# Kernel optimization log

Measured on AMD Instinct MI355X. Metric: run time of the kernel, lower is better.

The kernel has to match this reference:

```python
import jax, jax.numpy as jnp
import numpy as np

# Product-key memory config (matches init_kwargs)
HEADS = 4
K_DIM = 512          # per-head query/key dim; split in two halves of 256
HALF = K_DIM // 2
V_DIM = 512
SUBSIZE = 512        # sub-keys per bank; value table size = SUBSIZE**2
SIZE = SUBSIZE * SUBSIZE
TOPK = 8
TEMP = 1.0
B, T = 4, 2048


def setup_inputs() -> dict:
    key = jax.random.key(0)
    kq, kk, kv = jax.random.split(key, 3)
    bound = 1.0 / np.sqrt(K_DIM)  # reset_parameters: uniform(-1/sqrt(k_dim), 1/sqrt(k_dim))
    query = jax.random.normal(kq, (B, T, HEADS * K_DIM), dtype=jnp.float32)
    keys = jax.random.uniform(kk, (2 * HEADS * SUBSIZE, HALF), dtype=jnp.float32,
                              minval=-bound, maxval=bound)
    # reset_parameters: normal(0, v_dim**-0.5)
    values = jax.random.normal(kv, (SIZE, V_DIM), dtype=jnp.float32) * (V_DIM ** -0.5)
    return {"query": query, "keys": keys, "values": values}


def reference(query, keys, values):
    """retrieve_values: product-key two-stage topk + softmax-weighted embedding bag.
    query: [B, T, HEADS*K_DIM]; keys: [2*HEADS*SUBSIZE, HALF]; values: [SIZE, V_DIM]
    returns retrieved values [B*T, V_DIM].
    """
    Bq, Tq = query.shape[:2]
    N = Bq * Tq
    q = query.reshape(N, HEADS, K_DIM)
    q1, q2 = q[..., :HALF], q[..., HALF:]
    k = keys.reshape(2, HEADS, SUBSIZE, HALF)

    # Sub-key score matmuls (the two 'cdist-like' searches)
    s1 = jnp.einsum('nhd,hsd->nhs', q1, k[0])       # [N, H, SUBSIZE]
    s2 = jnp.einsum('nhd,hsd->nhs', q2, k[1])       # [N, H, SUBSIZE]

    ts1, ti1 = jax.lax.top_k(s1, TOPK)               # [N, H, TOPK]
    ts2, ti2 = jax.lax.top_k(s2, TOPK)

    # Cartesian combination of the two topk sets, then global topk
    comb = (ts1[..., :, None] + ts2[..., None, :]).reshape(N, HEADS, TOPK * TOPK)
    scores, flat_idx = jax.lax.top_k(comb, TOPK)     # [N, H, TOPK]
    sel1 = jnp.take_along_axis(ti1, flat_idx // TOPK, axis=-1)
    sel2 = jnp.take_along_axis(ti2, flat_idx % TOPK, axis=-1)
    indices = sel1 * SUBSIZE + sel2                  # global value-table indices [N, H, TOPK]

    # score_transform: softmax over heads*topk (score_nonlinear='softmax')
    w = jax.nn.softmax(scores.reshape(N, HEADS * TOPK) / TEMP, axis=-1)

    # xformers_embedding_bag: weighted gather-sum over the huge value table
    gathered = values[indices.reshape(N, HEADS * TOPK)]   # [N, H*TOPK, V_DIM]
    vals = jnp.einsum('nk,nkd->nd', w, gathered)          # [N, V_DIM]
    return vals
```

## Files before the change

### kernel.cpp

```cpp
#include <hip/hip_runtime.h>
#include <hip/hip_bf16.h>
#include <math.h>

typedef unsigned short u16;
typedef __attribute__((ext_vector_type(8))) short short8;
typedef __attribute__((ext_vector_type(4))) float f32x4;

#define N_TOK   8192
#define N_HEADS 4
#define KDIM    512
#define HALFD   256
#define VDIM    512
#define SUBK    512
#define NCAND   16

__device__ __forceinline__ u16 f2bf(float f) {
    unsigned u = __float_as_uint(f);
    u += 0x7fffu + ((u >> 16) & 1u);
    return (u16)(u >> 16);
}

__device__ __forceinline__ unsigned med3u(unsigned a, unsigned b, unsigned c) {
    unsigned d;
    asm("v_med3_u32 %0, %1, %2, %3" : "=v"(d) : "v"(a), "v"(b), "v"(c));
    return d;
}

__global__ void k_convert(const float* __restrict__ in, u16* __restrict__ out, int n4) {
    int i = blockIdx.x * blockDim.x + threadIdx.x;
    int stride = gridDim.x * blockDim.x;
    for (; i < n4; i += stride) {
        float4 v = ((const float4*)in)[i];
        unsigned a = (unsigned)f2bf(v.x) | ((unsigned)f2bf(v.y) << 16);
        unsigned b = (unsigned)f2bf(v.z) | ((unsigned)f2bf(v.w) << 16);
        ((uint2*)out)[i] = make_uint2(a, b);
    }
}

__global__ __launch_bounds__(256) void k_score_topk(
    const float* __restrict__ query,
    const u16* __restrict__ kb,
    int* __restrict__ cand)
{
    __shared__ unsigned sc[16 * 513];
    const int nb = blockIdx.x, h = blockIdx.y, half = blockIdx.z;
    const int tid = threadIdx.x;
    const int wave = tid >> 6, l = tid & 63;
    const int lr = l & 15, lk = l >> 4;

    const float* qbase = query + (size_t)(nb * 16 + lr) * (N_HEADS * KDIM)
                       + h * KDIM + half * HALFD + lk * 8;
    short8 a[8];
#pragma unroll
    for (int kf = 0; kf < 8; ++kf) {
        float4 q0 = *(const float4*)(qbase + kf * 32);
        float4 q1 = *(const float4*)(qbase + kf * 32 + 4);
        short8 t;
        t[0] = (short)f2bf(q0.x); t[1] = (short)f2bf(q0.y);
        t[2] = (short)f2bf(q0.z); t[3] = (short)f2bf(q0.w);
        t[4] = (short)f2bf(q1.x); t[5] = (short)f2bf(q1.y);
        t[6] = (short)f2bf(q1.z); t[7] = (short)f2bf(q1.w);
        a[kf] = t;
    }

    const u16* kbase = kb + (size_t)(half * N_HEADS + h) * SUBK * HALFD;
#pragma unroll
    for (int t = 0; t < 8; ++t) {
        const int st = wave * 8 + t;
        const u16* kp = kbase + (size_t)(st * 16 + lr) * HALFD + lk * 8;
        short8 b[8];
#pragma unroll
        for (int kf = 0; kf < 8; ++kf)
            b[kf] = *(const short8*)(kp + kf * 32);
        f32x4 acc = {0.f, 0.f, 0.f, 0.f};
#pragma unroll
        for (int kf = 0; kf < 8; ++kf)
            acc = __builtin_amdgcn_mfma_f32_16x16x32_bf16(a[kf], b[kf], acc, 0, 0, 0);
#pragma unroll
        for (int r = 0; r < 4; ++r) {
            unsigned ub = __float_as_uint(acc[r]);
            unsigned key = ub ^ ((unsigned)((int)ub >> 31) | 0x80000000u);
            key = (key & 0xFFFFFE00u) | (unsigned)(st * 16 + lr);
            sc[(lk * 4 + r) * 513 + st * 16 + lr] = key;
        }
    }
    __syncthreads();

    const int row = tid >> 4, sub = tid & 15;
    unsigned tv[NCAND];
#pragma unroll
    for (int j = 0; j < NCAND; ++j) tv[j] = 0u;
    const int base = row * 513 + sub;
#pragma unroll
    for (int t = 0; t < 32; ++t) {
        unsigned v = sc[base + (t << 4)];
#pragma unroll
        for (int j = NCAND - 1; j >= 1; --j)
            tv[j] = med3u(tv[j - 1], tv[j], v);
        tv[0] = (tv[0] > v) ? tv[0] : v;
    }

    unsigned keep = 0;
#pragma unroll
    for (int r = 0; r < NCAND; ++r) {
        unsigned w = tv[0];
#pragma unroll
        for (int d = 1; d < 16; d <<= 1) {
            unsigned o = __shfl_xor(w, d, 16);
            w = (o > w) ? o : w;
        }
        if (sub == r) keep = w;
        bool pop = (tv[0] == w);
#pragma unroll
        for (int j = 0; j < NCAND - 1; ++j) tv[j] = pop ? tv[j + 1] : tv[j];
        tv[NCAND - 1] = pop ? 0u : tv[NCAND - 1];
    }
    const int n = nb * 16 + row;
    cand[((size_t)n * 8 + (h * 2 + half)) * NCAND + sub] = (int)(keep & 0x1FFu);
}

__global__ __launch_bounds__(256) void k_select_gather(
    const float* __restrict__ query,
    const float* __restrict__ keys,
    const float* __restrict__ values,
    const int* __restrict__ cand,
    float* __restrict__ out)
{
    __shared__ double rv[8][16];
    __shared__ int    ri[8][16];
    __shared__ double tsv[8][8];
    __shared__ int    tsi[8][8];
    __shared__ double s_comb[32];
    __shared__ int    sgi[32];
    __shared__ float  wsm[32];
    __shared__ float  part[4][512];

    const int n = blockIdx.x;
    const int tid = threadIdx.x;

    {
        const int dot = tid >> 1, pt = tid & 1;
        const int g = dot >> 4, j = dot & 15;
        const int h = g >> 1, half = g & 1;
        const int sidx = cand[((size_t)n * 8 + g) * NCAND + j];
        const float* qrow = query + (size_t)n * (N_HEADS * KDIM) + h * KDIM + half * HALFD + pt * 128;
        const float* krow = keys + ((size_t)(half * N_HEADS + h) * SUBK + sidx) * HALFD + pt * 128;
        double a0 = 0, a1 = 0, a2 = 0, a3 = 0;
#pragma unroll 8
        for (int d = 0; d < 128; d += 4) {
            float4 qv = *(const float4*)(qrow + d);
            float4 kv = *(const float4*)(krow + d);
            a0 = fma((double)qv.x, (double)kv.x, a0);
            a1 = fma((double)qv.y, (double)kv.y, a1);
            a2 = fma((double)qv.z, (double)kv.z, a2);
            a3 = fma((double)qv.w, (double)kv.w, a3);
        }
        double s = (a0 + a1) + (a2 + a3);
        double o = __shfl_xor(s, 1);
        if (pt == 0) { rv[g][j] = s + o; ri[g][j] = sidx; }
    }
    __syncthreads();

    if (tid < 128) {
        const int g = tid >> 4, j = tid & 15;
        double v = rv[g][j];
        const int idx = ri[g][j];
        for (int r = 0; r < 8; ++r) {
            double bv = v; int bj = j;
#pragma unroll
            for (int d = 1; d < 16; d <<= 1) {
                double ov = __shfl_xor(bv, d, 16);
                int    oj = __shfl_xor(bj, d, 16);
                if (ov > bv || (ov == bv && oj < bj)) { bv = ov; bj = oj; }
            }
            int widx = __shfl(idx, bj, 16);
            if (j == r) { tsv[g][r] = bv; tsi[g][r] = widx; }
            if (j == bj) v = -1e300;
        }
    }
    __syncthreads();

    {
        const int h = tid >> 6, f = tid & 63;
        double c = tsv[h * 2][f >> 3] + tsv[h * 2 + 1][f & 7];
        for (int r = 0; r < 8; ++r) {
            double bv = c; int bf = f;
#pragma unroll
            for (int d = 1; d < 64; d <<= 1) {
                double ov = __shfl_xor(bv, d, 64);
                int    of = __shfl_xor(bf, d, 64);
                if (ov > bv || (ov == bv && of < bf)) { bv = ov; bf = of; }
            }
            if (f == r) {
                s_comb[h * 8 + r] = bv;
                sgi[h * 8 + r] = tsi[h * 2][bf >> 3] * SUBK + tsi[h * 2 + 1][bf & 7];
            }
            if (f == bf) c = -1e300;
        }
    }
    __syncthreads();

    if (tid < 32) {
        const int k = tid;
        double s = s_comb[k];
        double m = s;
#pragma unroll
        for (int d = 1; d < 32; d <<= 1) m = fmax(m, __shfl_xor(m, d, 32));
        float e = expf((float)(s - m));
        float sum = e;
#pragma unroll
        for (int d = 1; d < 32; d <<= 1) sum += __shfl_xor(sum, d, 32);
        wsm[k] = e / sum;
    }
    __syncthreads();

    {
        const int w = tid >> 6, lane = tid & 63;
        float4 acc0 = {0.f, 0.f, 0.f, 0.f};
        float4 acc1 = {0.f, 0.f, 0.f, 0.f};
#pragma unroll
        for (int b = 0; b < 2; ++b) {
            float4 v0[4], v1[4];
#pragma unroll
            for (int r = 0; r < 4; ++r) {
                const int k = w * 8 + b * 4 + r;
                const float* vr = values + (size_t)sgi[k] * VDIM;
                v0[r] = *(const float4*)(vr + lane * 4);
                v1[r] = *(const float4*)(vr + 256 + lane * 4);
            }
#pragma unroll
            for (int r = 0; r < 4; ++r) {
                const float wk = wsm[w * 8 + b * 4 + r];
                acc0.x = fmaf(wk, v0[r].x, acc0.x);
                acc0.y = fmaf(wk, v0[r].y, acc0.y);
                acc0.z = fmaf(wk, v0[r].z, acc0.z);
                acc0.w = fmaf(wk, v0[r].w, acc0.w);
                acc1.x = fmaf(wk, v1[r].x, acc1.x);
                acc1.y = fmaf(wk, v1[r].y, acc1.y);
                acc1.z = fmaf(wk, v1[r].z, acc1.z);
                acc1.w = fmaf(wk, v1[r].w, acc1.w);
            }
        }
        *(float4*)(&part[w][lane * 4]) = acc0;
        *(float4*)(&part[w][256 + lane * 4]) = acc1;
    }
    __syncthreads();

    {
        const int c = tid * 2;
        float s0 = part[0][c]     + part[1][c]     + part[2][c]     + part[3][c];
        float s1 = part[0][c + 1] + part[1][c + 1] + part[2][c + 1] + part[3][c + 1];
        ((float2*)(out + (size_t)n * VDIM))[tid] = make_float2(s0, s1);
    }
}

extern "C" void kernel_launch(void* const* d_in, const int* in_sizes, int n_in,
                              void* d_out, int out_size, void* d_ws, size_t ws_size,
                              hipStream_t stream) {
    const float* query  = (const float*)d_in[0];
    const float* keys   = (const float*)d_in[1];
    const float* values = (const float*)d_in[2];
    float* out = (float*)d_out;

    char* ws = (char*)d_ws;
    u16* kb   = (u16*)ws;
    int* cand = (int*)(ws + 2097152);

    k_convert<<<512, 256, 0, stream>>>(keys, kb, (2 * N_HEADS * SUBK * HALFD) / 4);

    dim3 gB(N_TOK / 16, N_HEADS, 2);
    k_score_topk<<<gB, 256, 0, stream>>>(query, kb, cand);

    k_select_gather<<<N_TOK, 256, 0, stream>>>(query, keys, values, cand, out);
}
```

Measured before the change: 387.8 us.

## Split select and gather into separate kernels with one wave per token

Moves the weighted value gather out of the per-token select kernel into its own kernel. In the new kernel each 64-lane wave handles one token, takes indices and weights through shuffles, and keeps 16 row loads in flight. This drops the shared-memory partial reduction and the barriers, and lets the gather run at its own occupancy. The cost is an extra launch and a small round trip of indices and weights through global memory.

```diff
diff --git a/kernel.cpp b/kernel.cpp
--- a/kernel.cpp
+++ b/kernel.cpp
@@ -119,12 +119,12 @@
     cand[((size_t)n * 8 + (h * 2 + half)) * NCAND + sub] = (int)(keep & 0x1FFu);
 }
 
-__global__ __launch_bounds__(256) void k_select_gather(
+__global__ __launch_bounds__(256) void k_select(
     const float* __restrict__ query,
     const float* __restrict__ keys,
-    const float* __restrict__ values,
     const int* __restrict__ cand,
-    float* __restrict__ out)
+    int* __restrict__ gout,
+    float* __restrict__ wout)
 {
     __shared__ double rv[8][16];
     __shared__ int    ri[8][16];
@@ -132,8 +132,6 @@
     __shared__ int    tsi[8][8];
     __shared__ double s_comb[32];
     __shared__ int    sgi[32];
-    __shared__ float  wsm[32];
-    __shared__ float  part[4][512];
 
     const int n = blockIdx.x;
     const int tid = threadIdx.x;
@@ -210,48 +208,54 @@
         float sum = e;
 #pragma unroll
         for (int d = 1; d < 32; d <<= 1) sum += __shfl_xor(sum, d, 32);
-        wsm[k] = e / sum;
-    }
-    __syncthreads();
-
-    {
-        const int w = tid >> 6, lane = tid & 63;
-        float4 acc0 = {0.f, 0.f, 0.f, 0.f};
-        float4 acc1 = {0.f, 0.f, 0.f, 0.f};
-#pragma unroll
-        for (int b = 0; b < 2; ++b) {
-            float4 v0[4], v1[4];
-#pragma unroll
-            for (int r = 0; r < 4; ++r) {
-                const int k = w * 8 + b * 4 + r;
-                const float* vr = values + (size_t)sgi[k] * VDIM;
-                v0[r] = *(const float4*)(vr + lane * 4);
-                v1[r] = *(const float4*)(vr + 256 + lane * 4);
-            }
-#pragma unroll
-            for (int r = 0; r < 4; ++r) {
-                const float wk = wsm[w * 8 + b * 4 + r];
-                acc0.x = fmaf(wk, v0[r].x, acc0.x);
-                acc0.y = fmaf(wk, v0[r].y, acc0.y);
-                acc0.z = fmaf(wk, v0[r].z, acc0.z);
-                acc0.w = fmaf(wk, v0[r].w, acc0.w);
-                acc1.x = fmaf(wk, v1[r].x, acc1.x);
-                acc1.y = fmaf(wk, v1[r].y, acc1.y);
-                acc1.z = fmaf(wk, v1[r].z, acc1.z);
-                acc1.w = fmaf(wk, v1[r].w, acc1.w);
-            }
-        }
-        *(float4*)(&part[w][lane * 4]) = acc0;
-        *(float4*)(&part[w][256 + lane * 4]) = acc1;
-    }
-    __syncthreads();
-
-    {
-        const int c = tid * 2;
-        float s0 = part[0][c]     + part[1][c]     + part[2][c]     + part[3][c];
-        float s1 = part[0][c + 1] + part[1][c + 1] + part[2][c + 1] + part[3][c + 1];
-        ((float2*)(out + (size_t)n * VDIM))[tid] = make_float2(s0, s1);
-    }
+        wout[(size_t)n * 32 + k] = e / sum;
+        gout[(size_t)n * 32 + k] = sgi[k];
+    }
+}
+
+__global__ __launch_bounds__(256) void k_gather(
+    const float* __restrict__ values,
+    const int* __restrict__ gidx,
+    const float* __restrict__ w,
+    float* __restrict__ out)
+{
+    const int tok = blockIdx.x * 4 + (threadIdx.x >> 6);
+    const int lane = threadIdx.x & 63;
+
+    float wv = 0.f; unsigned off = 0u;
+    if (lane < 32) {
+        wv  = w[(size_t)tok * 32 + lane];
+        off = (unsigned)gidx[(size_t)tok * 32 + lane] * (unsigned)VDIM;
+    }
+
+    float4 acc0 = {0.f, 0.f, 0.f, 0.f};
+    float4 acc1 = {0.f, 0.f, 0.f, 0.f};
+#pragma unroll
+    for (int kb = 0; kb < 32; kb += 8) {
+        float4 v0[8], v1[8];
+#pragma unroll
+        for (int r = 0; r < 8; ++r) {
+            unsigned o = (unsigned)__shfl((int)off, kb + r, 64);
+            const float* vr = values + (size_t)o;
+            v0[r] = *(const float4*)(vr + lane * 4);
+            v1[r] = *(const float4*)(vr + 256 + lane * 4);
+        }
+#pragma unroll
+        for (int r = 0; r < 8; ++r) {
+            const float wk = __shfl(wv, kb + r, 64);
+            acc0.x = fmaf(wk, v0[r].x, acc0.x);
+            acc0.y = fmaf(wk, v0[r].y, acc0.y);
+            acc0.z = fmaf(wk, v0[r].z, acc0.z);
+            acc0.w = fmaf(wk, v0[r].w, acc0.w);
+            acc1.x = fmaf(wk, v1[r].x, acc1.x);
+            acc1.y = fmaf(wk, v1[r].y, acc1.y);
+            acc1.z = fmaf(wk, v1[r].z, acc1.z);
+            acc1.w = fmaf(wk, v1[r].w, acc1.w);
+        }
+    }
+    float* orow = out + (size_t)tok * VDIM;
+    *(float4*)(orow + lane * 4) = acc0;
+    *(float4*)(orow + 256 + lane * 4) = acc1;
 }
 
 extern "C" void kernel_launch(void* const* d_in, const int* in_sizes, int n_in,
@@ -263,13 +267,16 @@
     float* out = (float*)d_out;
 
     char* ws = (char*)d_ws;
-    u16* kb   = (u16*)ws;
-    int* cand = (int*)(ws + 2097152);
+    u16* kb    = (u16*)ws;
+    int* cand  = (int*)(ws + 2097152);
+    int* gidxb = (int*)(ws + 2097152 + 4194304);
+    float* wb  = (float*)(ws + 2097152 + 4194304 + 1048576);
 
     k_convert<<<512, 256, 0, stream>>>(keys, kb, (2 * N_HEADS * SUBK * HALFD) / 4);
 
     dim3 gB(N_TOK / 16, N_HEADS, 2);
     k_score_topk<<<gB, 256, 0, stream>>>(query, kb, cand);
 
-    k_select_gather<<<N_TOK, 256, 0, stream>>>(query, keys, values, cand, out);
-}
+    k_select<<<N_TOK, 256, 0, stream>>>(query, keys, cand, gidxb, wb);
+    k_gather<<<N_TOK / 4, 256, 0, stream>>>(values, gidxb, wb, out);
+}
```

After: 416.3 us. +7.4%, slower.

## Fuse score/top-k and select/gather kernels into one per-16-token kernel

Applied to the files above, without the earlier changes.

Merges the sub-key scoring and candidate top-k kernel with the rescoring, softmax and value-gather kernel. Each block handles 16 tokens: it loops over the 8 head/half groups to build candidates in shared memory, then processes the 16 tokens one after another. This removes the global candidate buffer round trip and one launch. In exchange the grid shrinks to 512 blocks, and the latency-bound gather phase is serialized per token inside a block, which greatly cuts memory-level parallelism and occupancy.

```diff
diff --git a/kernel.cpp b/kernel.cpp
--- a/kernel.cpp
+++ b/kernel.cpp
@@ -37,95 +37,15 @@
     }
 }
 
-__global__ __launch_bounds__(256) void k_score_topk(
+__global__ __launch_bounds__(256, 2) void k_fused(
     const float* __restrict__ query,
-    const u16* __restrict__ kb,
-    int* __restrict__ cand)
+    const u16*  __restrict__ kb,
+    const float* __restrict__ keys,
+    const float* __restrict__ values,
+    float* __restrict__ out)
 {
     __shared__ unsigned sc[16 * 513];
-    const int nb = blockIdx.x, h = blockIdx.y, half = blockIdx.z;
-    const int tid = threadIdx.x;
-    const int wave = tid >> 6, l = tid & 63;
-    const int lr = l & 15, lk = l >> 4;
-
-    const float* qbase = query + (size_t)(nb * 16 + lr) * (N_HEADS * KDIM)
-                       + h * KDIM + half * HALFD + lk * 8;
-    short8 a[8];
-#pragma unroll
-    for (int kf = 0; kf < 8; ++kf) {
-        float4 q0 = *(const float4*)(qbase + kf * 32);
-        float4 q1 = *(const float4*)(qbase + kf * 32 + 4);
-        short8 t;
-        t[0] = (short)f2bf(q0.x); t[1] = (short)f2bf(q0.y);
-        t[2] = (short)f2bf(q0.z); t[3] = (short)f2bf(q0.w);
-        t[4] = (short)f2bf(q1.x); t[5] = (short)f2bf(q1.y);
-        t[6] = (short)f2bf(q1.z); t[7] = (short)f2bf(q1.w);
-        a[kf] = t;
-    }
-
-    const u16* kbase = kb + (size_t)(half * N_HEADS + h) * SUBK * HALFD;
-#pragma unroll
-    for (int t = 0; t < 8; ++t) {
-        const int st = wave * 8 + t;
-        const u16* kp = kbase + (size_t)(st * 16 + lr) * HALFD + lk * 8;
-        short8 b[8];
-#pragma unroll
-        for (int kf = 0; kf < 8; ++kf)
-            b[kf] = *(const short8*)(kp + kf * 32);
-        f32x4 acc = {0.f, 0.f, 0.f, 0.f};
-#pragma unroll
-        for (int kf = 0; kf < 8; ++kf)
-            acc = __builtin_amdgcn_mfma_f32_16x16x32_bf16(a[kf], b[kf], acc, 0, 0, 0);
-#pragma unroll
-        for (int r = 0; r < 4; ++r) {
-            unsigned ub = __float_as_uint(acc[r]);
-            unsigned key = ub ^ ((unsigned)((int)ub >> 31) | 0x80000000u);
-            key = (key & 0xFFFFFE00u) | (unsigned)(st * 16 + lr);
-            sc[(lk * 4 + r) * 513 + st * 16 + lr] = key;
-        }
-    }
-    __syncthreads();
-
-    const int row = tid >> 4, sub = tid & 15;
-    unsigned tv[NCAND];
-#pragma unroll
-    for (int j = 0; j < NCAND; ++j) tv[j] = 0u;
-    const int base = row * 513 + sub;
-#pragma unroll
-    for (int t = 0; t < 32; ++t) {
-        unsigned v = sc[base + (t << 4)];
-#pragma unroll
-        for (int j = NCAND - 1; j >= 1; --j)
-            tv[j] = med3u(tv[j - 1], tv[j], v);
-        tv[0] = (tv[0] > v) ? tv[0] : v;
-    }
-
-    unsigned keep = 0;
-#pragma unroll
-    for (int r = 0; r < NCAND; ++r) {
-        unsigned w = tv[0];
-#pragma unroll
-        for (int d = 1; d < 16; d <<= 1) {
-            unsigned o = __shfl_xor(w, d, 16);
-            w = (o > w) ? o : w;
-        }
-        if (sub == r) keep = w;
-        bool pop = (tv[0] == w);
-#pragma unroll
-        for (int j = 0; j < NCAND - 1; ++j) tv[j] = pop ? tv[j + 1] : tv[j];
-        tv[NCAND - 1] = pop ? 0u : tv[NCAND - 1];
-    }
-    const int n = nb * 16 + row;
-    cand[((size_t)n * 8 + (h * 2 + half)) * NCAND + sub] = (int)(keep & 0x1FFu);
-}
-
-__global__ __launch_bounds__(256) void k_select_gather(
-    const float* __restrict__ query,
-    const float* __restrict__ keys,
-    const float* __restrict__ values,
-    const int* __restrict__ cand,
-    float* __restrict__ out)
-{
+    __shared__ int    cnd[8][16][NCAND];
     __shared__ double rv[8][16];
     __shared__ int    ri[8][16];
     __shared__ double tsv[8][8];
@@ -135,122 +55,203 @@
     __shared__ float  wsm[32];
     __shared__ float  part[4][512];
 
-    const int n = blockIdx.x;
+    const int nb = blockIdx.x;
     const int tid = threadIdx.x;
-
-    {
-        const int dot = tid >> 1, pt = tid & 1;
-        const int g = dot >> 4, j = dot & 15;
+    const int wave = tid >> 6, l = tid & 63;
+    const int lr = l & 15, lk = l >> 4;
+
+    for (int g = 0; g < 8; ++g) {
         const int h = g >> 1, half = g & 1;
-        const int sidx = cand[((size_t)n * 8 + g) * NCAND + j];
-        const float* qrow = query + (size_t)n * (N_HEADS * KDIM) + h * KDIM + half * HALFD + pt * 128;
-        const float* krow = keys + ((size_t)(half * N_HEADS + h) * SUBK + sidx) * HALFD + pt * 128;
-        double a0 = 0, a1 = 0, a2 = 0, a3 = 0;
+
+        const float* qbase = query + (size_t)(nb * 16 + lr) * (N_HEADS * KDIM)
+                           + h * KDIM + half * HALFD + lk * 8;
+        short8 a[8];
+#pragma unroll
+        for (int kf = 0; kf < 8; ++kf) {
+            float4 q0 = *(const float4*)(qbase + kf * 32);
+            float4 q1 = *(const float4*)(qbase + kf * 32 + 4);
+            short8 t;
+            t[0] = (short)f2bf(q0.x); t[1] = (short)f2bf(q0.y);
+            t[2] = (short)f2bf(q0.z); t[3] = (short)f2bf(q0.w);
+            t[4] = (short)f2bf(q1.x); t[5] = (short)f2bf(q1.y);
+            t[6] = (short)f2bf(q1.z); t[7] = (short)f2bf(q1.w);
+            a[kf] = t;
+        }
+
+        const u16* kbase = kb + (size_t)(half * N_HEADS + h) * SUBK * HALFD;
+#pragma unroll
+        for (int t = 0; t < 8; ++t) {
+            const int st = wave * 8 + t;
+            const u16* kp = kbase + (size_t)(st * 16 + lr) * HALFD + lk * 8;
+            short8 b[8];
+#pragma unroll
+            for (int kf = 0; kf < 8; ++kf)
+                b[kf] = *(const short8*)(kp + kf * 32);
+            f32x4 acc = {0.f, 0.f, 0.f, 0.f};
+#pragma unroll
+            for (int kf = 0; kf < 8; ++kf)
+                acc = __builtin_amdgcn_mfma_f32_16x16x32_bf16(a[kf], b[kf], acc, 0, 0, 0);
+#pragma unroll
+            for (int r = 0; r < 4; ++r) {
+                unsigned ub = __float_as_uint(acc[r]);
+                unsigned key = ub ^ ((unsigned)((int)ub >> 31) | 0x80000000u);
+                key = (key & 0xFFFFFE00u) | (unsigned)(st * 16 + lr);
+                sc[(lk * 4 + r) * 513 + st * 16 + lr] = key;
+            }
+        }
+        __syncthreads();
+
+        const int row = tid >> 4, sub = tid & 15;
+        unsigned tv[NCAND];
+#pragma unroll
+        for (int j = 0; j < NCAND; ++j) tv[j] = 0u;
+        const int base = row * 513 + sub;
+#pragma unroll
+        for (int t = 0; t < 32; ++t) {
+            unsigned v = sc[base + (t << 4)];
+#pragma unroll
+            for (int j = NCAND - 1; j >= 1; --j)
+                tv[j] = med3u(tv[j - 1], tv[j], v);
+            tv[0] = (tv[0] > v) ? tv[0] : v;
+        }
+
+        unsigned keep = 0;
+#pragma unroll
+        for (int r = 0; r < NCAND; ++r) {
+            unsigned w = tv[0];
+#pragma unroll
+            for (int d = 1; d < 16; d <<= 1) {
+                unsigned o = __shfl_xor(w, d, 16);
+                w = (o > w) ? o : w;
+            }
+            if (sub == r) keep = w;
+            bool pop = (tv[0] == w);
+#pragma unroll
+            for (int j = 0; j < NCAND - 1; ++j) tv[j] = pop ? tv[j + 1] : tv[j];
+            tv[NCAND - 1] = pop ? 0u : tv[NCAND - 1];
+        }
+        cnd[g][row][sub] = (int)(keep & 0x1FFu);
+        __syncthreads();
+    }
+
+    for (int tt = 0; tt < 16; ++tt) {
+        const int n = nb * 16 + tt;
+
+        {
+            const int dot = tid >> 1, pt = tid & 1;
+            const int g = dot >> 4, j = dot & 15;
+            const int h = g >> 1, half = g & 1;
+            const int sidx = cnd[g][tt][j];
+            const float* qrow = query + (size_t)n * (N_HEADS * KDIM) + h * KDIM + half * HALFD + pt * 128;
+            const float* krow = keys + ((size_t)(half * N_HEADS + h) * SUBK + sidx) * HALFD + pt * 128;
+            double a0 = 0, a1 = 0, a2 = 0, a3 = 0;
 #pragma unroll 8
-        for (int d = 0; d < 128; d += 4) {
-            float4 qv = *(const float4*)(qrow + d);
-            float4 kv = *(const float4*)(krow + d);
-            a0 = fma((double)qv.x, (double)kv.x, a0);
-            a1 = fma((double)qv.y, (double)kv.y, a1);
-            a2 = fma((double)qv.z, (double)kv.z, a2);
-            a3 = fma((double)qv.w, (double)kv.w, a3);
-        }
-        double s = (a0 + a1) + (a2 + a3);
-        double o = __shfl_xor(s, 1);
-        if (pt == 0) { rv[g][j] = s + o; ri[g][j] = sidx; }
-    }
-    __syncthreads();
-
-    if (tid < 128) {
-        const int g = tid >> 4, j = tid & 15;
-        double v = rv[g][j];
-        const int idx = ri[g][j];
-        for (int r = 0; r < 8; ++r) {
-            double bv = v; int bj = j;
-#pragma unroll
-            for (int d = 1; d < 16; d <<= 1) {
-                double ov = __shfl_xor(bv, d, 16);
-                int    oj = __shfl_xor(bj, d, 16);
-                if (ov > bv || (ov == bv && oj < bj)) { bv = ov; bj = oj; }
-            }
-            int widx = __shfl(idx, bj, 16);
-            if (j == r) { tsv[g][r] = bv; tsi[g][r] = widx; }
-            if (j == bj) v = -1e300;
-        }
-    }
-    __syncthreads();
-
-    {
-        const int h = tid >> 6, f = tid & 63;
-        double c = tsv[h * 2][f >> 3] + tsv[h * 2 + 1][f & 7];
-        for (int r = 0; r < 8; ++r) {
-            double bv = c; int bf = f;
-#pragma unroll
-            for (int d = 1; d < 64; d <<= 1) {
-                double ov = __shfl_xor(bv, d, 64);
-                int    of = __shfl_xor(bf, d, 64);
-                if (ov > bv || (ov == bv && of < bf)) { bv = ov; bf = of; }
-            }
-            if (f == r) {
-                s_comb[h * 8 + r] = bv;
-                sgi[h * 8 + r] = tsi[h * 2][bf >> 3] * SUBK + tsi[h * 2 + 1][bf & 7];
-            }
-            if (f == bf) c = -1e300;
-        }
-    }
-    __syncthreads();
-
-    if (tid < 32) {
-        const int k = tid;
-        double s = s_comb[k];
-        double m = s;
-#pragma unroll
-        for (int d = 1; d < 32; d <<= 1) m = fmax(m, __shfl_xor(m, d, 32));
-        float e = expf((float)(s - m));
-        float sum = e;
-#pragma unroll
-        for (int d = 1; d < 32; d <<= 1) sum += __shfl_xor(sum, d, 32);
-        wsm[k] = e / sum;
-    }
-    __syncthreads();
-
-    {
-        const int w = tid >> 6, lane = tid & 63;
-        float4 acc0 = {0.f, 0.f, 0.f, 0.f};
-        float4 acc1 = {0.f, 0.f, 0.f, 0.f};
-#pragma unroll
-        for (int b = 0; b < 2; ++b) {
-            float4 v0[4], v1[4];
-#pragma unroll
-            for (int r = 0; r < 4; ++r) {
-                const int k = w * 8 + b * 4 + r;
-                const float* vr = values + (size_t)sgi[k] * VDIM;
-                v0[r] = *(const float4*)(vr + lane * 4);
-                v1[r] = *(const float4*)(vr + 256 + lane * 4);
-            }
-#pragma unroll
-            for (int r = 0; r < 4; ++r) {
-                const float wk = wsm[w * 8 + b * 4 + r];
-                acc0.x = fmaf(wk, v0[r].x, acc0.x);
-                acc0.y = fmaf(wk, v0[r].y, acc0.y);
-                acc0.z = fmaf(wk, v0[r].z, acc0.z);
-                acc0.w = fmaf(wk, v0[r].w, acc0.w);
-                acc1.x = fmaf(wk, v1[r].x, acc1.x);
-                acc1.y = fmaf(wk, v1[r].y, acc1.y);
-                acc1.z = fmaf(wk, v1[r].z, acc1.z);
-                acc1.w = fmaf(wk, v1[r].w, acc1.w);
-            }
-        }
-        *(float4*)(&part[w][lane * 4]) = acc0;
-        *(float4*)(&part[w][256 + lane * 4]) = acc1;
-    }
-    __syncthreads();
-
-    {
-        const int c = tid * 2;
-        float s0 = part[0][c]     + part[1][c]     + part[2][c]     + part[3][c];
-        float s1 = part[0][c + 1] + part[1][c + 1] + part[2][c + 1] + part[3][c + 1];
-        ((float2*)(out + (size_t)n * VDIM))[tid] = make_float2(s0, s1);
+            for (int d = 0; d < 128; d += 4) {
+                float4 qv = *(const float4*)(qrow + d);
+                float4 kv = *(const float4*)(krow + d);
+                a0 = fma((double)qv.x, (double)kv.x, a0);
+                a1 = fma((double)qv.y, (double)kv.y, a1);
+                a2 = fma((double)qv.z, (double)kv.z, a2);
+                a3 = fma((double)qv.w, (double)kv.w, a3);
+            }
+            double s = (a0 + a1) + (a2 + a3);
+            double o = __shfl_xor(s, 1);
+            if (pt == 0) { rv[g][j] = s + o; ri[g][j] = sidx; }
+        }
+        __syncthreads();
+
+        if (tid < 128) {
+            const int g = tid >> 4, j = tid & 15;
+            double v = rv[g][j];
+            const int idx = ri[g][j];
+            for (int r = 0; r < 8; ++r) {
+                double bv = v; int bj = j;
+#pragma unroll
+                for (int d = 1; d < 16; d <<= 1) {
+                    double ov = __shfl_xor(bv, d, 16);
+                    int    oj = __shfl_xor(bj, d, 16);
+                    if (ov > bv || (ov == bv && oj < bj)) { bv = ov; bj = oj; }
+                }
+                int widx = __shfl(idx, bj, 16);
+                if (j == r) { tsv[g][r] = bv; tsi[g][r] = widx; }
+                if (j == bj) v = -1e300;
+            }
+        }
+        __syncthreads();
+
+        {
+            const int h = tid >> 6, f = tid & 63;
+            double c = tsv[h * 2][f >> 3] + tsv[h * 2 + 1][f & 7];
+            for (int r = 0; r < 8; ++r) {
+                double bv = c; int bf = f;
+#pragma unroll
+                for (int d = 1; d < 64; d <<= 1) {
+                    double ov = __shfl_xor(bv, d, 64);
+                    int    of = __shfl_xor(bf, d, 64);
+                    if (ov > bv || (ov == bv && of < bf)) { bv = ov; bf = of; }
+                }
+                if (f == r) {
+                    s_comb[h * 8 + r] = bv;
+                    sgi[h * 8 + r] = tsi[h * 2][bf >> 3] * SUBK + tsi[h * 2 + 1][bf & 7];
+                }
+                if (f == bf) c = -1e300;
+            }
+        }
+        __syncthreads();
+
+        if (tid < 32) {
+            const int k = tid;
+            double s = s_comb[k];
+            double m = s;
+#pragma unroll
+            for (int d = 1; d < 32; d <<= 1) m = fmax(m, __shfl_xor(m, d, 32));
+            float e = expf((float)(s - m));
+            float sum = e;
+#pragma unroll
+            for (int d = 1; d < 32; d <<= 1) sum += __shfl_xor(sum, d, 32);
+            wsm[k] = e / sum;
+        }
+        __syncthreads();
+
+        {
+            const int w = wave, lane = l;
+            float4 acc0 = {0.f, 0.f, 0.f, 0.f};
+            float4 acc1 = {0.f, 0.f, 0.f, 0.f};
+#pragma unroll
+            for (int b = 0; b < 2; ++b) {
+                float4 v0[4], v1[4];
+#pragma unroll
+                for (int r = 0; r < 4; ++r) {
+                    const int k = w * 8 + b * 4 + r;
+                    const float* vr = values + (size_t)sgi[k] * VDIM;
+                    v0[r] = *(const float4*)(vr + lane * 4);
+                    v1[r] = *(const float4*)(vr + 256 + lane * 4);
+                }
+#pragma unroll
+                for (int r = 0; r < 4; ++r) {
+                    const float wk = wsm[w * 8 + b * 4 + r];
+                    acc0.x = fmaf(wk, v0[r].x, acc0.x);
+                    acc0.y = fmaf(wk, v0[r].y, acc0.y);
+                    acc0.z = fmaf(wk, v0[r].z, acc0.z);
+                    acc0.w = fmaf(wk, v0[r].w, acc0.w);
+                    acc1.x = fmaf(wk, v1[r].x, acc1.x);
+                    acc1.y = fmaf(wk, v1[r].y, acc1.y);
+                    acc1.z = fmaf(wk, v1[r].z, acc1.z);
+                    acc1.w = fmaf(wk, v1[r].w, acc1.w);
+                }
+            }
+            *(float4*)(&part[w][lane * 4]) = acc0;
+            *(float4*)(&part[w][256 + lane * 4]) = acc1;
+        }
+        __syncthreads();
+
+        {
+            const int c = tid * 2;
+            float s0 = part[0][c]     + part[1][c]     + part[2][c]     + part[3][c];
+            float s1 = part[0][c + 1] + part[1][c + 1] + part[2][c + 1] + part[3][c + 1];
+            ((float2*)(out + (size_t)n * VDIM))[tid] = make_float2(s0, s1);
+        }
+        __syncthreads();
     }
 }
 
@@ -263,13 +264,9 @@
     float* out = (float*)d_out;
 
     char* ws = (char*)d_ws;
-    u16* kb   = (u16*)ws;
-    int* cand = (int*)(ws + 2097152);
+    u16* kb = (u16*)ws;
 
     k_convert<<<512, 256, 0, stream>>>(keys, kb, (2 * N_HEADS * SUBK * HALFD) / 4);
 
-    dim3 gB(N_TOK / 16, N_HEADS, 2);
-    k_score_topk<<<gB, 256, 0, stream>>>(query, kb, cand);
-
-    k_select_gather<<<N_TOK, 256, 0, stream>>>(query, keys, values, cand, out);
-}
+    k_fused<<<N_TOK / 16, 256, 0, stream>>>(query, kb, keys, values, out);
+}
```

Result: slower. 486.5 us (+25.5%).
